# Kernel tuning notes

Measured on AMD Instinct MI355X. Metric: run time of the kernel, lower is better.

The kernel has to match this reference:

```python
import jax, jax.numpy as jnp
import numpy as np
from jax import lax

H = 192; W = 192; C = 256; N = H * W; E = 294912; K = 289; DSIG = 1
SLOPE = 0.01
EPS = 1e-5


def leaky(x):
    return jnp.where(x >= 0, x, SLOPE * x)


def conv2d(x, w, pad, groups):
    return lax.conv_general_dilated(
        x, w, (1, 1), [(pad, pad), (pad, pad)],
        dimension_numbers=('NCHW', 'OIHW', 'NCHW'),
        feature_group_count=groups)


def bn2d(x, g, b):
    # BatchNorm2d with track_running_stats=False -> always batch stats (biased var)
    m = x.mean(axis=(0, 2, 3), keepdims=True)
    v = x.var(axis=(0, 2, 3), keepdims=True)
    return (x - m) / jnp.sqrt(v + EPS) * g.reshape(1, -1, 1, 1) + b.reshape(1, -1, 1, 1)


def conv_batch(x, w, g, b, pad, groups):
    # nn.Sequential(LeakyReLU(0.01), Conv2d(bias=False), BatchNorm2d)
    return bn2d(conv2d(leaky(x), w, pad, groups), g, b)


def bn1d(x, g, b):
    m = x.mean(axis=0)
    v = x.var(axis=0)
    return (x - m) / jnp.sqrt(v + EPS) * g + b


def setup_inputs() -> dict:
    key = jax.random.key(0)
    ks = jax.random.split(key, 20)
    X = jax.random.normal(ks[0], (N, C), dtype=jnp.float32)
    src = jax.random.randint(ks[1], (E,), 0, N)
    dst = jax.random.randint(ks[2], (E,), 0, N)
    k1 = jax.random.randint(ks[3], (E,), 0, K)
    k2 = jax.random.randint(ks[4], (E,), 0, K)
    InfoIdx = jnp.stack([src, k1, dst, k2], axis=1).astype(jnp.int64)
    edgmsk = (jax.random.uniform(ks[5], (E, 1)) < 0.9).astype(jnp.float32)
    s = 0.05
    inp = {
        'X': X, 'InfoIdx': InfoIdx, 'edgmsk': edgmsk,
        # PPM: depthwise 17x17 conv_batch then 1x1 conv_batch
        'ppm_w0': jax.random.normal(ks[6], (C, 1, 17, 17), jnp.float32) * s,
        'ppm_g0': jnp.ones((C,), jnp.float32), 'ppm_b0': jnp.zeros((C,), jnp.float32),
        'ppm_w1': jax.random.normal(ks[7], (C, C, 1, 1), jnp.float32) * s,
        'ppm_g1': jnp.ones((C,), jnp.float32), 'ppm_b1': jnp.zeros((C,), jnp.float32),
        # FFN_1: two 1x1 conv_batch
        'ffn1_w0': jax.random.normal(ks[8], (C, C, 1, 1), jnp.float32) * s,
        'ffn1_g0': jnp.ones((C,), jnp.float32), 'ffn1_b0': jnp.zeros((C,), jnp.float32),
        'ffn1_w1': jax.random.normal(ks[9], (C, C, 1, 1), jnp.float32) * s,
        'ffn1_g1': jnp.ones((C,), jnp.float32), 'ffn1_b1': jnp.zeros((C,), jnp.float32),
        # Dis: Linear(C,C) -> LeakyReLU -> Linear(C, 289)
        'dis_w1': jax.random.normal(ks[10], (C, C), jnp.float32) * s,
        'dis_b1': jnp.zeros((C,), jnp.float32),
        'dis_w2': jax.random.normal(ks[11], (K * DSIG, C), jnp.float32) * s,
        'dis_b2': jnp.zeros((K * DSIG,), jnp.float32),
        # BatchNorm1d
        'bn_g': jnp.ones((C,), jnp.float32), 'bn_b': jnp.zeros((C,), jnp.float32),
        # FFN_2 = DoubleConv: depthwise-expand 3x3 (groups=C, out=4C) then 1x1
        'ffn2_w0': jax.random.normal(ks[12], (4 * C, 1, 3, 3), jnp.float32) * s,
        'ffn2_g0': jnp.ones((4 * C,), jnp.float32), 'ffn2_b0': jnp.zeros((4 * C,), jnp.float32),
        'ffn2_w1': jax.random.normal(ks[13], (C, 4 * C, 1, 1), jnp.float32) * s,
        'ffn2_g1': jnp.ones((C,), jnp.float32), 'ffn2_b1': jnp.zeros((C,), jnp.float32),
    }
    return inp


def reference(X, InfoIdx, edgmsk,
              ppm_w0, ppm_g0, ppm_b0, ppm_w1, ppm_g1, ppm_b1,
              ffn1_w0, ffn1_g0, ffn1_b0, ffn1_w1, ffn1_g1, ffn1_b1,
              dis_w1, dis_b1, dis_w2, dis_b2, bn_g, bn_b,
              ffn2_w0, ffn2_g0, ffn2_b0, ffn2_w1, ffn2_g1, ffn2_b1):
    src_idx = InfoIdx[:, 0]
    dst_idx = InfoIdx[:, 2]
    # [N,C] -> [1,C,H,W]
    img = X.T.reshape(1, C, H, W)
    # PPM residual
    t = conv_batch(img, ppm_w0, ppm_g0, ppm_b0, pad=8, groups=C)
    t = conv_batch(t, ppm_w1, ppm_g1, ppm_b1, pad=0, groups=1)
    img = img + t
    # FFN_1 residual
    t = conv_batch(img, ffn1_w0, ffn1_g0, ffn1_b0, pad=0, groups=1)
    t = conv_batch(t, ffn1_w1, ffn1_g1, ffn1_b1, pad=0, groups=1)
    img = img + t
    Xn = img.reshape(C, N).T  # [N, C]
    # Dis MLP -> signal [N, 289, d_signal]
    h = leaky(Xn @ dis_w1.T + dis_b1)
    signal = (h @ dis_w2.T + dis_b2).reshape(N, K, DSIG)
    # edge gather + exp/clamp score
    s_src = signal[src_idx, InfoIdx[:, 1]]  # [E, 1]
    s_dst = signal[dst_idx, InfoIdx[:, 3]]  # [E, 1]
    aij = jnp.exp(jnp.clip(s_src + s_dst, -5.0, 5.0)) * edgmsk  # [E, 1]
    # two scatter-sum reductions to dst nodes
    A_sum = jax.ops.segment_sum(aij, dst_idx, num_segments=N)  # [N, 1]
    XA_sum = jax.ops.segment_sum(Xn[src_idx] * aij, dst_idx, num_segments=N)  # [N, C]
    X_trans = XA_sum / (A_sum + 1e-5)
    Xn = Xn + bn1d(X_trans, bn_g, bn_b)
    # FFN_2 = DoubleConv with residual skip
    img = Xn.T.reshape(1, C, H, W)
    t = conv_batch(img, ffn2_w0, ffn2_g0, ffn2_b0, pad=1, groups=C)
    t = conv_batch(t, ffn2_w1, ffn2_g1, ffn2_b1, pad=0, groups=1)
    out = t + img
    return out.reshape(C, N).T  # final bg.ndata['X'], [N, C]
```

## Files before the change

kernel.cpp:

```cpp
#include <hip/hip_runtime.h>
#include <cstddef>

#define HW 192
#define NP 36864
#define CH 256
#define EDGES 294912
#define KSIG 289
#define SLOPE 0.01f
#define BNEPS 1e-5f
#define PADW 208
#define PADSZ (PADW * PADW)

typedef unsigned short u16;
typedef __attribute__((ext_vector_type(8))) short bf16x8;
typedef __attribute__((ext_vector_type(4))) float f32x4;

__device__ __forceinline__ float leaky(float x) { return x >= 0.f ? x : SLOPE * x; }
__device__ __forceinline__ u16 f2bf(float x) {
  unsigned u = __float_as_uint(x);
  unsigned r = (u + 0x7fffu + ((u >> 16) & 1u)) >> 16;
  return (u16)r;
}
__device__ __forceinline__ float bf2f(unsigned h) { return __uint_as_float(h << 16); }
__device__ __forceinline__ void bnss(const float* sums, const float* sqs,
                                     const float* g, const float* b, int k,
                                     float& s, float& h) {
  float mean = sums[k] * (1.f / NP);
  float var = sqs[k] * (1.f / NP) - mean * mean;
  s = g[k] * rsqrtf(var + BNEPS);
  h = b[k] - mean * s;
}

__global__ __launch_bounds__(256) void k_transpose_pad(const float* __restrict__ src,
                                                       float* __restrict__ dst,
                                                       u16* __restrict__ pad) {
  __shared__ float tile[32][33];
  int s0 = blockIdx.x * 32, r0 = blockIdx.y * 32;
  int tx = threadIdx.x & 31, ty = threadIdx.x >> 5;
#pragma unroll
  for (int j = 0; j < 4; j++)
    tile[ty + 8 * j][tx] = src[(size_t)(r0 + ty + 8 * j) * CH + s0 + tx];
  __syncthreads();
  int n = r0 + tx;
  int y = n / HW, x = n - y * HW;
#pragma unroll
  for (int j = 0; j < 4; j++) {
    int c = s0 + ty + 8 * j;
    float v = tile[tx][ty + 8 * j];
    dst[(size_t)c * NP + n] = v;
    pad[(size_t)c * PADSZ + (y + 8) * PADW + x + 8] = f2bf(leaky(v));
  }
}

__global__ __launch_bounds__(256) void k_mkT(const float* __restrict__ w,
                                             u16* __restrict__ Tg) {
  int c = blockIdx.x;
  const float* wc = w + c * 289;
  u16* tc = Tg + (size_t)c * 8704;
  for (int i = threadIdx.x; i < 8704; i += 256) {
    int ky = i >> 9, rem = i & 511, n = rem >> 5, k = rem & 31;
    int kx = k - n;
    float v = (kx >= 0 && kx < 17) ? wc[ky * 17 + kx] : 0.f;
    tc[i] = f2bf(v);
  }
}

__global__ __launch_bounds__(256) void k_cvtW(const float* __restrict__ pw1,
                                              const float* __restrict__ f1w0,
                                              const float* __restrict__ f1w1,
                                              const float* __restrict__ dw1,
                                              const float* __restrict__ dw2,
                                              const float* __restrict__ f2w1,
                                              u16* __restrict__ out) {
  int i = blockIdx.x * 256 + threadIdx.x;
  float v;
  if (i < 65536) v = pw1[i];
  else if (i < 131072) v = f1w0[i - 65536];
  else if (i < 196608) v = f1w1[i - 131072];
  else if (i < 262144) v = dw1[i - 196608];
  else if (i < 360448) { int j = i - 262144; v = (j < KSIG * 256) ? dw2[j] : 0.f; }
  else v = f2w1[i - 360448];
  out[i] = f2bf(v);
}

__global__ __launch_bounds__(256) void k_stats_bf(const u16* __restrict__ Xr,
                                                  float* __restrict__ sums,
                                                  float* __restrict__ sqs) {
  int row = blockIdx.x;
  int t = threadIdx.x;
  const uint4* p = (const uint4*)(Xr + (size_t)row * NP);
  float s = 0.f, q = 0.f;
  for (int i = t; i < NP / 8; i += 256) {
    uint4 v = p[i];
    unsigned w[4] = {v.x, v.y, v.z, v.w};
#pragma unroll
    for (int j = 0; j < 4; j++) {
      float a = bf2f(w[j] & 0xffffu), c = bf2f(w[j] >> 16);
      s += a + c; q += a * a + c * c;
    }
  }
  __shared__ float ss[256], qq[256];
  ss[t] = s; qq[t] = q;
  __syncthreads();
  for (int d = 128; d > 0; d >>= 1) {
    if (t < d) { ss[t] += ss[t + d]; qq[t] += qq[t + d]; }
    __syncthreads();
  }
  if (t == 0) { sums[row] = ss[0]; sqs[row] = qq[0]; }
}

__global__ __launch_bounds__(256) void k_cvtT(const float* __restrict__ in,
                                              u16* __restrict__ outT, int M) {
  __shared__ float tile[32][65];
  int n0 = blockIdx.x * 64, k0 = blockIdx.y * 32;
  int t = threadIdx.x;
#pragma unroll
  for (int i = 0; i < 2; i++) {
    int ci = i * 256 + t;
    int k = ci >> 4, cg = (ci & 15) * 4;
    float4 v = *(const float4*)&in[(size_t)(k0 + k) * NP + n0 + cg];
    tile[k][cg] = v.x; tile[k][cg + 1] = v.y; tile[k][cg + 2] = v.z; tile[k][cg + 3] = v.w;
  }
  __syncthreads();
  int n = t >> 2, kg = (t & 3) * 8;
  uint4 o;
  o.x = (unsigned)f2bf(tile[kg + 0][n]) | ((unsigned)f2bf(tile[kg + 1][n]) << 16);
  o.y = (unsigned)f2bf(tile[kg + 2][n]) | ((unsigned)f2bf(tile[kg + 3][n]) << 16);
  o.z = (unsigned)f2bf(tile[kg + 4][n]) | ((unsigned)f2bf(tile[kg + 5][n]) << 16);
  o.w = (unsigned)f2bf(tile[kg + 6][n]) | ((unsigned)f2bf(tile[kg + 7][n]) << 16);
  *(uint4*)&outT[(size_t)(n0 + n) * M + k0 + kg] = o;
}

__global__ __launch_bounds__(256) void k_cvtT_bf(const u16* __restrict__ in,
                                                 u16* __restrict__ outT,
                                                 const float* __restrict__ sums,
                                                 const float* __restrict__ sqs,
                                                 const float* __restrict__ g,
                                                 const float* __restrict__ b, int M) {
  __shared__ float tile[32][65];
  int n0 = blockIdx.x * 64, k0 = blockIdx.y * 32;
  int t = threadIdx.x;
  int k = t >> 3, cg = (t & 7) * 8;
  float s, h; bnss(sums, sqs, g, b, k0 + k, s, h);
  uint4 v = *(const uint4*)&in[(size_t)(k0 + k) * NP + n0 + cg];
  unsigned w[4] = {v.x, v.y, v.z, v.w};
#pragma unroll
  for (int j = 0; j < 4; j++) {
    tile[k][cg + 2 * j]     = leaky(fmaf(bf2f(w[j] & 0xffffu), s, h));
    tile[k][cg + 2 * j + 1] = leaky(fmaf(bf2f(w[j] >> 16), s, h));
  }
  __syncthreads();
  int n = t >> 2, kg = (t & 3) * 8;
  uint4 o;
  o.x = (unsigned)f2bf(tile[kg + 0][n]) | ((unsigned)f2bf(tile[kg + 1][n]) << 16);
  o.y = (unsigned)f2bf(tile[kg + 2][n]) | ((unsigned)f2bf(tile[kg + 3][n]) << 16);
  o.z = (unsigned)f2bf(tile[kg + 4][n]) | ((unsigned)f2bf(tile[kg + 5][n]) << 16);
  o.w = (unsigned)f2bf(tile[kg + 6][n]) | ((unsigned)f2bf(tile[kg + 7][n]) << 16);
  *(uint4*)&outT[(size_t)(n0 + n) * M + k0 + kg] = o;
}

__global__ __launch_bounds__(256) void k_fuse1(const float* __restrict__ base,
                                               const u16* __restrict__ raw,
                                               const float* __restrict__ sums,
                                               const float* __restrict__ sqs,
                                               const float* __restrict__ g,
                                               const float* __restrict__ b,
                                               float* __restrict__ img2,
                                               u16* __restrict__ outT) {
  __shared__ float tile[32][65];
  int n0 = blockIdx.x * 64, k0 = blockIdx.y * 32;
  int t = threadIdx.x;
#pragma unroll
  for (int i = 0; i < 2; i++) {
    int ci = i * 256 + t;
    int k = ci >> 4, cg = (ci & 15) * 4;
    float s, h; bnss(sums, sqs, g, b, k0 + k, s, h);
    size_t idx = (size_t)(k0 + k) * NP + n0 + cg;
    float4 bv = *(const float4*)&base[idx];
    uint2 rv = *(const uint2*)&raw[idx];
    float r0 = bf2f(rv.x & 0xffffu), r1 = bf2f(rv.x >> 16);
    float r2 = bf2f(rv.y & 0xffffu), r3 = bf2f(rv.y >> 16);
    float4 o;
    o.x = bv.x + fmaf(r0, s, h); o.y = bv.y + fmaf(r1, s, h);
    o.z = bv.z + fmaf(r2, s, h); o.w = bv.w + fmaf(r3, s, h);
    *(float4*)&img2[idx] = o;
    tile[k][cg]     = leaky(o.x);
    tile[k][cg + 1] = leaky(o.y);
    tile[k][cg + 2] = leaky(o.z);
    tile[k][cg + 3] = leaky(o.w);
  }
  __syncthreads();
  int n = t >> 2, kg = (t & 3) * 8;
  uint4 o;
  o.x = (unsigned)f2bf(tile[kg + 0][n]) | ((unsigned)f2bf(tile[kg + 1][n]) << 16);
  o.y = (unsigned)f2bf(tile[kg + 2][n]) | ((unsigned)f2bf(tile[kg + 3][n]) << 16);
  o.z = (unsigned)f2bf(tile[kg + 4][n]) | ((unsigned)f2bf(tile[kg + 5][n]) << 16);
  o.w = (unsigned)f2bf(tile[kg + 6][n]) | ((unsigned)f2bf(tile[kg + 7][n]) << 16);
  *(uint4*)&outT[(size_t)(n0 + n) * CH + k0 + kg] = o;
}

__global__ __launch_bounds__(256) void k_fuse2(const float* __restrict__ base,
                                               const u16* __restrict__ raw,
                                               const float* __restrict__ sums,
                                               const float* __restrict__ sqs,
                                               const float* __restrict__ g,
                                               const float* __restrict__ b,
                                               float* __restrict__ XnT,
                                               u16* __restrict__ outT) {
  __shared__ float tile[32][65];
  int n0 = blockIdx.x * 64, k0 = blockIdx.y * 32;
  int t = threadIdx.x;
#pragma unroll
  for (int i = 0; i < 2; i++) {
    int ci = i * 256 + t;
    int k = ci >> 4, cg = (ci & 15) * 4;
    float s, h; bnss(sums, sqs, g, b, k0 + k, s, h);
    size_t idx = (size_t)(k0 + k) * NP + n0 + cg;
    float4 bv = *(const float4*)&base[idx];
    uint2 rv = *(const uint2*)&raw[idx];
    float r0 = bf2f(rv.x & 0xffffu), r1 = bf2f(rv.x >> 16);
    float r2 = bf2f(rv.y & 0xffffu), r3 = bf2f(rv.y >> 16);
    tile[k][cg]     = bv.x + fmaf(r0, s, h);
    tile[k][cg + 1] = bv.y + fmaf(r1, s, h);
    tile[k][cg + 2] = bv.z + fmaf(r2, s, h);
    tile[k][cg + 3] = bv.w + fmaf(r3, s, h);
  }
  __syncthreads();
  int n = t >> 2, kg = (t & 3) * 8;
  float4 f0 = {tile[kg + 0][n], tile[kg + 1][n], tile[kg + 2][n], tile[kg + 3][n]};
  float4 f1 = {tile[kg + 4][n], tile[kg + 5][n], tile[kg + 6][n], tile[kg + 7][n]};
  *(float4*)&XnT[(size_t)(n0 + n) * CH + k0 + kg] = f0;
  *(float4*)&XnT[(size_t)(n0 + n) * CH + k0 + kg + 4] = f1;
  uint4 o;
  o.x = (unsigned)f2bf(f0.x) | ((unsigned)f2bf(f0.y) << 16);
  o.y = (unsigned)f2bf(f0.z) | ((unsigned)f2bf(f0.w) << 16);
  o.z = (unsigned)f2bf(f1.x) | ((unsigned)f2bf(f1.y) << 16);
  o.w = (unsigned)f2bf(f1.z) | ((unsigned)f2bf(f1.w) << 16);
  *(uint4*)&outT[(size_t)(n0 + n) * CH + k0 + kg] = o;
}

__global__ __launch_bounds__(256) void k_mgemm(const u16* __restrict__ A,
                                               const u16* __restrict__ Bt,
                                               float* __restrict__ Outf,
                                               u16* __restrict__ Outb,
                                               const float* __restrict__ bias,
                                               int K, int Mstore, int actout) {
  __shared__ u16 As[128 * 40];
  __shared__ u16 Bs[128 * 40];
  int t = threadIdx.x;
  int lane = t & 63, wave = t >> 6;
  int wm = (wave >> 1) * 64, wn = (wave & 1) * 64;
  int m0 = blockIdx.y * 128, n0 = blockIdx.x * 128;
  int r = lane & 15, q = lane >> 4;
  f32x4 acc[4][4];
#pragma unroll
  for (int a = 0; a < 4; a++)
#pragma unroll
    for (int b = 0; b < 4; b++) acc[a][b] = (f32x4){0.f, 0.f, 0.f, 0.f};

  for (int k0 = 0; k0 < K; k0 += 32) {
#pragma unroll
    for (int i = 0; i < 2; i++) {
      int cc = t + i * 256;
      int mm = cc >> 2, kq = (cc & 3) * 8;
      uint4 av = *(const uint4*)&A[(size_t)(m0 + mm) * K + k0 + kq];
      uint4 bv = *(const uint4*)&Bt[(size_t)(n0 + mm) * K + k0 + kq];
      *(uint4*)&As[mm * 40 + kq] = av;
      *(uint4*)&Bs[mm * 40 + kq] = bv;
    }
    __syncthreads();
    bf16x8 af[4], bfr[4];
#pragma unroll
    for (int mt = 0; mt < 4; mt++)
      af[mt] = *(const bf16x8*)&As[(wm + mt * 16 + r) * 40 + q * 8];
#pragma unroll
    for (int nt = 0; nt < 4; nt++)
      bfr[nt] = *(const bf16x8*)&Bs[(wn + nt * 16 + r) * 40 + q * 8];
#pragma unroll
    for (int mt = 0; mt < 4; mt++)
#pragma unroll
      for (int nt = 0; nt < 4; nt++)
        acc[mt][nt] = __builtin_amdgcn_mfma_f32_16x16x32_bf16(af[mt], bfr[nt], acc[mt][nt], 0, 0, 0);
    __syncthreads();
  }
#pragma unroll
  for (int mt = 0; mt < 4; mt++) {
    int mrow = m0 + wm + mt * 16 + q * 4;
#pragma unroll
    for (int i = 0; i < 4; i++) {
      int m = mrow + i;
      if (m >= Mstore) continue;
      float bs = bias ? bias[m] : 0.f;
#pragma unroll
      for (int nt = 0; nt < 4; nt++) {
        float v = acc[mt][nt][i] + bs;
        if (actout) v = leaky(v);
        size_t oi = (size_t)m * NP + n0 + wn + nt * 16 + r;
        if (Outb) Outb[oi] = f2bf(v); else Outf[oi] = v;
      }
    }
  }
}

__global__ __launch_bounds__(512) void k_mgemm256(const u16* __restrict__ A,
                                                  const u16* __restrict__ Bt,
                                                  float* __restrict__ Outf,
                                                  u16* __restrict__ Outb,
                                                  const float* __restrict__ bias,
                                                  int K, int actout) {
  __shared__ u16 As[256 * 40];
  __shared__ u16 Bs[128 * 40];
  int t = threadIdx.x;
  int lane = t & 63, wave = t >> 6;
  int wm = (wave >> 1) * 64, wn = (wave & 1) * 64;
  int n0 = blockIdx.x * 128;
  int r = lane & 15, q = lane >> 4;
  int arow0 = t >> 2, kq = (t & 3) * 8;
  f32x4 acc[4][4];
#pragma unroll
  for (int a = 0; a < 4; a++)
#pragma unroll
    for (int b = 0; b < 4; b++) acc[a][b] = (f32x4){0.f, 0.f, 0.f, 0.f};

  uint4 pa0, pa1, pb;
  pa0 = *(const uint4*)&A[(size_t)arow0 * K + kq];
  pa1 = *(const uint4*)&A[(size_t)(arow0 + 128) * K + kq];
  pb  = *(const uint4*)&Bt[(size_t)(n0 + arow0) * K + kq];
  int kiters = K >> 5;
  for (int ki = 0; ki < kiters; ki++) {
    *(uint4*)&As[arow0 * 40 + kq] = pa0;
    *(uint4*)&As[(arow0 + 128) * 40 + kq] = pa1;
    *(uint4*)&Bs[arow0 * 40 + kq] = pb;
    __syncthreads();
    if (ki + 1 < kiters) {
      int k0 = (ki + 1) << 5;
      pa0 = *(const uint4*)&A[(size_t)arow0 * K + k0 + kq];
      pa1 = *(const uint4*)&A[(size_t)(arow0 + 128) * K + k0 + kq];
      pb  = *(const uint4*)&Bt[(size_t)(n0 + arow0) * K + k0 + kq];
    }
    bf16x8 af[4], bfr[4];
#pragma unroll
    for (int mt = 0; mt < 4; mt++)
      af[mt] = *(const bf16x8*)&As[(wm + mt * 16 + r) * 40 + q * 8];
#pragma unroll
    for (int nt = 0; nt < 4; nt++)
      bfr[nt] = *(const bf16x8*)&Bs[(wn + nt * 16 + r) * 40 + q * 8];
#pragma unroll
    for (int mt = 0; mt < 4; mt++)
#pragma unroll
      for (int nt = 0; nt < 4; nt++)
        acc[mt][nt] = __builtin_amdgcn_mfma_f32_16x16x32_bf16(af[mt], bfr[nt], acc[mt][nt], 0, 0, 0);
    __syncthreads();
  }
#pragma unroll
  for (int mt = 0; mt < 4; mt++) {
    int mrow = wm + mt * 16 + q * 4;
#pragma unroll
    for (int i = 0; i < 4; i++) {
      int m = mrow + i;
      float bs = bias ? bias[m] : 0.f;
#pragma unroll
      for (int nt = 0; nt < 4; nt++) {
        float v = acc[mt][nt][i] + bs;
        if (actout) v = leaky(v);
        size_t oi = (size_t)m * NP + n0 + wn + nt * 16 + r;
        if (Outb) Outb[oi] = f2bf(v); else Outf[oi] = v;
      }
    }
  }
}

__global__ __launch_bounds__(256) void k_dwconv17(const u16* __restrict__ pad,
                                                  const u16* __restrict__ Tg,
                                                  u16* __restrict__ outb) {
  int c = blockIdx.y;
  int tile = blockIdx.x;
  int ty0 = (tile / 3) * 64, tx0 = (tile % 3) * 64;
  __shared__ u16 smIn[80 * 88];
  __shared__ u16 smT[17 * 16 * 40];
  const u16* pc = pad + (size_t)c * PADSZ;
  for (int cc = threadIdx.x; cc < 800; cc += 256) {
    int rr = cc / 10, j = cc - rr * 10;
    uint4 v = *(const uint4*)(pc + (ty0 + rr) * PADW + tx0 + j * 8);
    *(uint4*)(smIn + rr * 88 + j * 8) = v;
  }
  const u16* tc = Tg + (size_t)c * 8704;
  for (int cc = threadIdx.x; cc < 1088; cc += 256) {
    int rr = cc >> 2, j = cc & 3;
    uint4 v = *(const uint4*)(tc + rr * 32 + j * 8);
    *(uint4*)(smT + rr * 40 + j * 8) = v;
  }
  __syncthreads();
  int lane = threadIdx.x & 63, wave = threadIdx.x >> 6;
  int wy = wave * 16;
  int r = lane & 15, q = lane >> 4;
  f32x4 acc[4];
#pragma unroll
  for (int xt = 0; xt < 4; xt++) acc[xt] = (f32x4){0.f, 0.f, 0.f, 0.f};
#pragma unroll
  for (int ky = 0; ky < 17; ky++) {
    bf16x8 bfrag = *(const bf16x8*)&smT[(ky * 16 + r) * 40 + q * 8];
    int rowA = wy + r + ky;
#pragma unroll
    for (int xt = 0; xt < 4; xt++) {
      bf16x8 afrag = *(const bf16x8*)&smIn[rowA * 88 + xt * 16 + q * 8];
      acc[xt] = __builtin_amdgcn_mfma_f32_16x16x32_bf16(afrag, bfrag, acc[xt], 0, 0, 0);
    }
  }
  u16* oc = outb + (size_t)c * NP;
#pragma unroll
  for (int xt = 0; xt < 4; xt++) {
    int x = tx0 + xt * 16 + r;
#pragma unroll
    for (int i = 0; i < 4; i++) {
      int y = ty0 + wy + q * 4 + i;
      oc[y * HW + x] = f2bf(acc[xt][i]);
    }
  }
}

__global__ __launch_bounds__(256) void k_conv3x4(const float* __restrict__ in,
                                                 const float* __restrict__ w,
                                                 u16* __restrict__ out) {
  int wave = threadIdx.x >> 6, lane = threadIdx.x & 63;
  int c = blockIdx.y;
  int y = blockIdx.x * 4 + wave;
  const float* wc = w + (size_t)(4 * c) * 9;
  float wr[36];
#pragma unroll
  for (int k = 0; k < 36; k++) wr[k] = wc[k];
  float acc[4][3];
#pragma unroll
  for (int oc = 0; oc < 4; oc++)
#pragma unroll
    for (int s = 0; s < 3; s++) acc[oc][s] = 0.f;
  const float* base = in + (size_t)c * NP;
#pragma unroll
  for (int ky = 0; ky < 3; ky++) {
    int ry = y + ky - 1;
    if (ry < 0 || ry >= HW) continue;
    const float* rp = base + ry * HW;
    float a0 = leaky(rp[lane]);
    float a1 = leaky(rp[64 + lane]);
    float a2 = leaky(rp[128 + lane]);
    float e0 = __shfl(a0, 63), e1 = __shfl(a1, 63);
    float b1 = __shfl(a1, 0),  b2 = __shfl(a2, 0);
    float l0 = __shfl_up(a0, 1); if (lane == 0) l0 = 0.f;
    float l1 = __shfl_up(a1, 1); if (lane == 0) l1 = e0;
    float l2 = __shfl_up(a2, 1); if (lane == 0) l2 = e1;
    float r0 = __shfl_down(a0, 1); if (lane == 63) r0 = b1;
    float r1 = __shfl_down(a1, 1); if (lane == 63) r1 = b2;
    float r2 = __shfl_down(a2, 1); if (lane == 63) r2 = 0.f;
#pragma unroll
    for (int oc = 0; oc < 4; oc++) {
      float w0 = wr[oc * 9 + ky * 3], w1 = wr[oc * 9 + ky * 3 + 1], w2 = wr[oc * 9 + ky * 3 + 2];
      acc[oc][0] = fmaf(w0, l0, fmaf(w1, a0, fmaf(w2, r0, acc[oc][0])));
      acc[oc][1] = fmaf(w0, l1, fmaf(w1, a1, fmaf(w2, r1, acc[oc][1])));
      acc[oc][2] = fmaf(w0, l2, fmaf(w1, a2, fmaf(w2, r2, acc[oc][2])));
    }
  }
  size_t ob = (size_t)(4 * c) * NP + (size_t)y * HW + lane;
#pragma unroll
  for (int oc = 0; oc < 4; oc++) {
    out[ob + (size_t)oc * NP]       = f2bf(acc[oc][0]);
    out[ob + (size_t)oc * NP + 64]  = f2bf(acc[oc][1]);
    out[ob + (size_t)oc * NP + 128] = f2bf(acc[oc][2]);
  }
}

__global__ __launch_bounds__(256) void k_edge(const int* __restrict__ info,
                                              const float* __restrict__ msk,
                                              const float* __restrict__ sig,
                                              float* __restrict__ aij,
                                              int* __restrict__ counts) {
  int e = blockIdx.x * 256 + threadIdx.x;
  int4 ii = ((const int4*)info)[e];
  float s = sig[(size_t)ii.y * NP + ii.x] + sig[(size_t)ii.w * NP + ii.z];
  s = fminf(fmaxf(s, -5.f), 5.f);
  aij[e] = expf(s) * msk[e];
  atomicAdd(&counts[ii.z], 1);
}

__global__ __launch_bounds__(256) void k_scan1(const int* __restrict__ counts,
                                               int* __restrict__ offsets,
                                               int* __restrict__ bsum) {
  __shared__ int sm[256];
  int t = threadIdx.x;
  int i = blockIdx.x * 256 + t;
  int v = counts[i];
  sm[t] = v;
  __syncthreads();
  for (int d = 1; d < 256; d <<= 1) {
    int add = (t >= d) ? sm[t - d] : 0;
    __syncthreads();
    sm[t] += add;
    __syncthreads();
  }
  offsets[i] = sm[t] - v;
  if (t == 255) bsum[blockIdx.x] = sm[255];
}
__global__ __launch_bounds__(256) void k_scan2(const int* __restrict__ bsum,
                                               int* __restrict__ boff) {
  __shared__ int sm[256];
  int t = threadIdx.x;
  int v = (t < 144) ? bsum[t] : 0;
  sm[t] = v;
  __syncthreads();
  for (int d = 1; d < 256; d <<= 1) {
    int add = (t >= d) ? sm[t - d] : 0;
    __syncthreads();
    sm[t] += add;
    __syncthreads();
  }
  boff[t] = sm[t] - v;
}
__global__ __launch_bounds__(256) void k_scan3(int* __restrict__ offsets,
                                               const int* __restrict__ boff,
                                               int* __restrict__ cursor) {
  int i = blockIdx.x * 256 + threadIdx.x;
  int o = offsets[i] + boff[blockIdx.x];
  offsets[i] = o;
  cursor[i] = o;
  if (i == 0) offsets[NP] = EDGES;
}
__global__ __launch_bounds__(256) void k_scatter(const int* __restrict__ info,
                                                 const float* __restrict__ aij,
                                                 int* __restrict__ cursor,
                                                 int* __restrict__ srcs,
                                                 float* __restrict__ aijw) {
  int e = blockIdx.x * 256 + threadIdx.x;
  int4 ii = ((const int4*)info)[e];
  int pos = atomicAdd(&cursor[ii.z], 1);
  srcs[pos] = ii.x;
  aijw[pos] = aij[e];
}

__global__ __launch_bounds__(256) void k_agg(const int* __restrict__ offsets,
                                             const int* __restrict__ srcs,
                                             const float* __restrict__ aijw,
                                             const u16* __restrict__ XnBf,
                                             u16* __restrict__ XtrBf) {
  int wave = threadIdx.x >> 6, lane = threadIdx.x & 63;
  int node = blockIdx.x * 4 + wave;
  int o0 = offsets[node], o1 = offsets[node + 1];
  int half = lane >> 5, l32 = lane & 31;
  float acc[8] = {0.f, 0.f, 0.f, 0.f, 0.f, 0.f, 0.f, 0.f};
  float asum = 0.f;
  int i = o0 + half;
  for (; i + 2 < o1; i += 4) {
    int s0 = srcs[i], s1 = srcs[i + 2];
    float a0 = aijw[i], a1 = aijw[i + 2];
    uint4 v0 = ((const uint4*)(XnBf + (size_t)s0 * CH))[l32];
    uint4 v1 = ((const uint4*)(XnBf + (size_t)s1 * CH))[l32];
    unsigned w0[4] = {v0.x, v0.y, v0.z, v0.w};
    unsigned w1[4] = {v1.x, v1.y, v1.z, v1.w};
#pragma unroll
    for (int j = 0; j < 4; j++) {
      acc[2 * j]     = fmaf(a0, bf2f(w0[j] & 0xffffu), acc[2 * j]);
      acc[2 * j + 1] = fmaf(a0, bf2f(w0[j] >> 16),     acc[2 * j + 1]);
      acc[2 * j]     = fmaf(a1, bf2f(w1[j] & 0xffffu), acc[2 * j]);
      acc[2 * j + 1] = fmaf(a1, bf2f(w1[j] >> 16),     acc[2 * j + 1]);
    }
    asum += a0 + a1;
  }
  for (; i < o1; i += 2) {
    int s = srcs[i];
    float a = aijw[i];
    uint4 v = ((const uint4*)(XnBf + (size_t)s * CH))[l32];
    unsigned w[4] = {v.x, v.y, v.z, v.w};
#pragma unroll
    for (int j = 0; j < 4; j++) {
      acc[2 * j]     = fmaf(a, bf2f(w[j] & 0xffffu), acc[2 * j]);
      acc[2 * j + 1] = fmaf(a, bf2f(w[j] >> 16),     acc[2 * j + 1]);
    }
    asum += a;
  }
#pragma unroll
  for (int j = 0; j < 8; j++) acc[j] += __shfl_xor(acc[j], 32, 64);
  asum += __shfl_xor(asum, 32, 64);
  if (half == 0) {
    float inv = 1.f / (asum + 1e-5f);
    uint4 o;
    o.x = (unsigned)f2bf(acc[0] * inv) | ((unsigned)f2bf(acc[1] * inv) << 16);
    o.y = (unsigned)f2bf(acc[2] * inv) | ((unsigned)f2bf(acc[3] * inv) << 16);
    o.z = (unsigned)f2bf(acc[4] * inv) | ((unsigned)f2bf(acc[5] * inv) << 16);
    o.w = (unsigned)f2bf(acc[6] * inv) | ((unsigned)f2bf(acc[7] * inv) << 16);
    ((uint4*)(XtrBf + (size_t)node * CH))[l32] = o;
  }
}

__global__ __launch_bounds__(256) void k_colstats(const u16* __restrict__ Xt,
                                                  float* __restrict__ sums,
                                                  float* __restrict__ sqs) {
  int c = threadIdx.x;
  float s = 0.f, q = 0.f;
  for (int n = blockIdx.x; n < NP; n += gridDim.x) {
    float v = bf2f(Xt[(size_t)n * CH + c]);
    s += v; q += v * v;
  }
  atomicAdd(&sums[c], s);
  atomicAdd(&sqs[c], q);
}

__global__ __launch_bounds__(256) void k_mkimg4(const float* __restrict__ Xn,
                                                const u16* __restrict__ XtrBf,
                                                const float* __restrict__ sums,
                                                const float* __restrict__ sqs,
                                                const float* __restrict__ g,
                                                const float* __restrict__ b,
                                                float* __restrict__ img4) {
  __shared__ float tile[32][33];
  int c0 = blockIdx.x * 32, n0 = blockIdx.y * 32;
  int tx = threadIdx.x & 31, ty = threadIdx.x >> 5;
  int c = c0 + tx;
  float s, h; bnss(sums, sqs, g, b, c, s, h);
#pragma unroll
  for (int j = 0; j < 4; j++) {
    size_t idx = (size_t)(n0 + ty + 8 * j) * CH + c;
    tile[ty + 8 * j][tx] = Xn[idx] + fmaf(bf2f(XtrBf[idx]), s, h);
  }
  __syncthreads();
#pragma unroll
  for (int j = 0; j < 4; j++) {
    int cc = c0 + ty + 8 * j;
    img4[(size_t)cc * NP + n0 + tx] = tile[tx][ty + 8 * j];
  }
}

__global__ __launch_bounds__(256) void k_final(const u16* __restrict__ raw5,
                                               const float* __restrict__ img4,
                                               const float* __restrict__ sums,
                                               const float* __restrict__ sqs,
                                               const float* __restrict__ g,
                                               const float* __restrict__ b,
                                               float* __restrict__ out) {
  __shared__ float tile[32][33];
  int n0 = blockIdx.x * 32, c0 = blockIdx.y * 32;
  int tx = threadIdx.x & 31, ty = threadIdx.x >> 5;
#pragma unroll
  for (int j = 0; j < 4; j++) {
    int c = c0 + ty + 8 * j;
    float s, h; bnss(sums, sqs, g, b, c, s, h);
    size_t idx = (size_t)c * NP + n0 + tx;
    tile[ty + 8 * j][tx] = fmaf(bf2f(raw5[idx]), s, h) + img4[idx];
  }
  __syncthreads();
#pragma unroll
  for (int j = 0; j < 4; j++) {
    int n = n0 + ty + 8 * j;
    out[(size_t)n * CH + c0 + tx] = tile[tx][ty + 8 * j];
  }
}

extern "C" void kernel_launch(void* const* d_in, const int* in_sizes, int n_in,
                              void* d_out, int out_size, void* d_ws, size_t ws_size,
                              hipStream_t stream) {
  (void)in_sizes; (void)n_in; (void)out_size; (void)ws_size;
  const float* X    = (const float*)d_in[0];
  const int*   info = (const int*)d_in[1];
  const float* msk  = (const float*)d_in[2];
  const float* pw0  = (const float*)d_in[3];
  const float* pg0  = (const float*)d_in[4];
  const float* pb0  = (const float*)d_in[5];
  const float* pw1  = (const float*)d_in[6];
  const float* pg1  = (const float*)d_in[7];
  const float* pb1  = (const float*)d_in[8];
  const float* f1w0 = (const float*)d_in[9];
  const float* f1g0 = (const float*)d_in[10];
  const float* f1b0 = (const float*)d_in[11];
  const float* f1w1 = (const float*)d_in[12];
  const float* f1g1 = (const float*)d_in[13];
  const float* f1b1 = (const float*)d_in[14];
  const float* dw1  = (const float*)d_in[15];
  const float* db1  = (const float*)d_in[16];
  const float* dw2  = (const float*)d_in[17];
  const float* db2  = (const float*)d_in[18];
  const float* bng  = (const float*)d_in[19];
  const float* bnb  = (const float*)d_in[20];
  const float* f2w0 = (const float*)d_in[21];
  const float* f2g0 = (const float*)d_in[22];
  const float* f2b0 = (const float*)d_in[23];
  const float* f2w1 = (const float*)d_in[24];
  const float* f2g1 = (const float*)d_in[25];
  const float* f2b1 = (const float*)d_in[26];
  float* out = (float*)d_out;

  float* ws = (float*)d_ws;
  float* sum0 = ws + 0;    float* sq0 = ws + 256;
  float* sum1 = ws + 512;  float* sq1 = ws + 768;
  float* sum2 = ws + 1024; float* sq2 = ws + 1280;
  float* sum3 = ws + 1536; float* sq3 = ws + 1792;
  float* sum5 = ws + 2048; float* sq5 = ws + 2304;
  float* sumT = ws + 2560; float* sqT = ws + 2816;
  float* sum4 = ws + 3072; float* sq4 = ws + 4096;
  int* counts  = (int*)(ws + 8192);
  int* offsets = (int*)(ws + 45056);
  int* cursor  = (int*)(ws + 82176);
  int* bsum    = (int*)(ws + 119296);
  int* boff    = (int*)(ws + 119552);
  int* srcs    = (int*)(ws + 131072);
  float* aij   = ws + 425984;
  const size_t S = (size_t)NP * CH;
  float* slotD = ws + 720896;
  float* slotB = slotD + S;
  float* slotA = slotB + S;
  float* slotC = slotA + S;
  u16* bfB  = (u16*)(slotC + S);
  u16* bfH  = bfB + S;
  float* sigT = (float*)(bfH + S);
  u16* bfW  = (u16*)(sigT + (size_t)KSIG * NP);
  float* aijw = (float*)(bfW + 622592);
  u16* Ppad = (u16*)slotC;
  u16* Tg   = (u16*)slotD;
  u16* raw4bf  = (u16*)slotB;
  u16* bfT1024 = bfB;
  u16* XtrBf   = (u16*)slotD;
  u16* raw5bf  = (u16*)slotB;

  hipMemsetAsync(ws, 0, 5120 * sizeof(float), stream);
  hipMemsetAsync(counts, 0, NP * sizeof(int), stream);
  hipMemsetAsync(Ppad, 0, (size_t)PADSZ * CH * sizeof(u16), stream);

  dim3 b256(256), b512(512);
  k_cvtW<<<2432, b256, 0, stream>>>(pw1, f1w0, f1w1, dw1, dw2, f2w1, bfW);
  k_mkT<<<CH, b256, 0, stream>>>(pw0, Tg);
  k_transpose_pad<<<dim3(CH / 32, NP / 32), b256, 0, stream>>>(X, slotA, Ppad);
  k_dwconv17<<<dim3(9, CH), b256, 0, stream>>>(Ppad, Tg, bfH);
  k_stats_bf<<<CH, b256, 0, stream>>>(bfH, sum0, sq0);
  k_cvtT_bf<<<dim3(NP / 64, 8), b256, 0, stream>>>(bfH, bfB, sum0, sq0, pg0, pb0, CH);
  k_mgemm256<<<NP / 128, b512, 0, stream>>>(bfW, bfB, nullptr, bfH, nullptr, CH, 0);
  k_stats_bf<<<CH, b256, 0, stream>>>(bfH, sum1, sq1);
  k_fuse1<<<dim3(NP / 64, 8), b256, 0, stream>>>(slotA, bfH, sum1, sq1, pg1, pb1, slotD, bfB);
  k_mgemm256<<<NP / 128, b512, 0, stream>>>(bfW + 65536, bfB, nullptr, bfH, nullptr, CH, 0);
  k_stats_bf<<<CH, b256, 0, stream>>>(bfH, sum2, sq2);
  k_cvtT_bf<<<dim3(NP / 64, 8), b256, 0, stream>>>(bfH, bfB, sum2, sq2, f1g0, f1b0, CH);
  k_mgemm256<<<NP / 128, b512, 0, stream>>>(bfW + 131072, bfB, nullptr, bfH, nullptr, CH, 0);
  k_stats_bf<<<CH, b256, 0, stream>>>(bfH, sum3, sq3);
  k_fuse2<<<dim3(NP / 64, 8), b256, 0, stream>>>(slotD, bfH, sum3, sq3, f1g1, f1b1, slotA, bfB);
  k_mgemm256<<<NP / 128, b512, 0, stream>>>(bfW + 196608, bfB, slotC, nullptr, db1, CH, 1);
  k_cvtT<<<dim3(NP / 64, 8), b256, 0, stream>>>(slotC, bfH, CH);
  k_mgemm<<<dim3(NP / 128, 3), b256, 0, stream>>>(bfW + 262144, bfH, sigT, nullptr, db2, CH, KSIG, 0);
  k_edge<<<EDGES / 256, b256, 0, stream>>>(info, msk, sigT, aij, counts);
  k_scan1<<<NP / 256, b256, 0, stream>>>(counts, offsets, bsum);
  k_scan2<<<1, b256, 0, stream>>>(bsum, boff);
  k_scan3<<<NP / 256, b256, 0, stream>>>(offsets, boff, cursor);
  k_scatter<<<EDGES / 256, b256, 0, stream>>>(info, aij, cursor, srcs, aijw);
  k_agg<<<NP / 4, b256, 0, stream>>>(offsets, srcs, aijw, bfB, XtrBf);
  k_colstats<<<288, b256, 0, stream>>>(XtrBf, sumT, sqT);
  k_mkimg4<<<dim3(CH / 32, NP / 32), b256, 0, stream>>>(slotA, XtrBf, sumT, sqT, bng, bnb, slotC);
  k_conv3x4<<<dim3(48, CH), b256, 0, stream>>>(slotC, f2w0, raw4bf);
  k_stats_bf<<<1024, b256, 0, stream>>>(raw4bf, sum4, sq4);
  k_cvtT_bf<<<dim3(NP / 64, 32), b256, 0, stream>>>(raw4bf, bfT1024, sum4, sq4, f2g0, f2b0, 1024);
  k_mgemm256<<<NP / 128, b512, 0, stream>>>(bfW + 360448, bfT1024, nullptr, raw5bf, nullptr, 1024, 0);
  k_stats_bf<<<CH, b256, 0, stream>>>(raw5bf, sum5, sq5);
  k_final<<<dim3(NP / 32, CH / 32), b256, 0, stream>>>(raw5bf, slotC, sum5, sq5, f2g1, f2b1, out);
}
```

Measured before the change: 642.9 us.

## Fuse BN statistics into conv and GEMM epilogues, halve GEMM N-tile

Batch-norm sums and sums of squares are now accumulated with wave shuffles and atomics in the epilogues of the depthwise conv, the 3x3 conv, and the 1x1 GEMMs. This removes the separate stats kernels that re-read each activation tensor. The GEMM tile is narrowed to 64 columns for more blocks and occupancy. Stats are now taken from fp32 values rather than rounded bf16, and float atomics make the sums order-nondeterministic.

```diff
diff --git a/kernel.cpp b/kernel.cpp
--- a/kernel.cpp
+++ b/kernel.cpp
@@ -81,32 +81,6 @@
   else if (i < 360448) { int j = i - 262144; v = (j < KSIG * 256) ? dw2[j] : 0.f; }
   else v = f2w1[i - 360448];
   out[i] = f2bf(v);
-}
-
-__global__ __launch_bounds__(256) void k_stats_bf(const u16* __restrict__ Xr,
-                                                  float* __restrict__ sums,
-                                                  float* __restrict__ sqs) {
-  int row = blockIdx.x;
-  int t = threadIdx.x;
-  const uint4* p = (const uint4*)(Xr + (size_t)row * NP);
-  float s = 0.f, q = 0.f;
-  for (int i = t; i < NP / 8; i += 256) {
-    uint4 v = p[i];
-    unsigned w[4] = {v.x, v.y, v.z, v.w};
-#pragma unroll
-    for (int j = 0; j < 4; j++) {
-      float a = bf2f(w[j] & 0xffffu), c = bf2f(w[j] >> 16);
-      s += a + c; q += a * a + c * c;
-    }
-  }
-  __shared__ float ss[256], qq[256];
-  ss[t] = s; qq[t] = q;
-  __syncthreads();
-  for (int d = 128; d > 0; d >>= 1) {
-    if (t < d) { ss[t] += ss[t + d]; qq[t] += qq[t + d]; }
-    __syncthreads();
-  }
-  if (t == 0) { sums[row] = ss[0]; sqs[row] = qq[0]; }
 }
 
 __global__ __launch_bounds__(256) void k_cvtT(const float* __restrict__ in,
@@ -302,69 +276,78 @@
   }
 }
 
-__global__ __launch_bounds__(512) void k_mgemm256(const u16* __restrict__ A,
-                                                  const u16* __restrict__ Bt,
-                                                  float* __restrict__ Outf,
-                                                  u16* __restrict__ Outb,
-                                                  const float* __restrict__ bias,
-                                                  int K, int actout) {
+__global__ __launch_bounds__(512, 4) void k_mgemm256(const u16* __restrict__ A,
+                                                     const u16* __restrict__ Bt,
+                                                     float* __restrict__ Outf,
+                                                     u16* __restrict__ Outb,
+                                                     const float* __restrict__ bias,
+                                                     int K, int actout,
+                                                     float* __restrict__ sums,
+                                                     float* __restrict__ sqs) {
   __shared__ u16 As[256 * 40];
-  __shared__ u16 Bs[128 * 40];
+  __shared__ u16 Bs[64 * 40];
   int t = threadIdx.x;
   int lane = t & 63, wave = t >> 6;
-  int wm = (wave >> 1) * 64, wn = (wave & 1) * 64;
-  int n0 = blockIdx.x * 128;
+  int wm = (wave >> 1) * 64, wn = (wave & 1) * 32;
+  int n0 = blockIdx.x * 64;
   int r = lane & 15, q = lane >> 4;
   int arow0 = t >> 2, kq = (t & 3) * 8;
-  f32x4 acc[4][4];
+  int brow = t >> 2;
+  f32x4 acc[4][2];
 #pragma unroll
   for (int a = 0; a < 4; a++)
 #pragma unroll
-    for (int b = 0; b < 4; b++) acc[a][b] = (f32x4){0.f, 0.f, 0.f, 0.f};
+    for (int b = 0; b < 2; b++) acc[a][b] = (f32x4){0.f, 0.f, 0.f, 0.f};
 
   uint4 pa0, pa1, pb;
   pa0 = *(const uint4*)&A[(size_t)arow0 * K + kq];
   pa1 = *(const uint4*)&A[(size_t)(arow0 + 128) * K + kq];
-  pb  = *(const uint4*)&Bt[(size_t)(n0 + arow0) * K + kq];
+  if (t < 256) pb = *(const uint4*)&Bt[(size_t)(n0 + brow) * K + kq];
   int kiters = K >> 5;
   for (int ki = 0; ki < kiters; ki++) {
     *(uint4*)&As[arow0 * 40 + kq] = pa0;
     *(uint4*)&As[(arow0 + 128) * 40 + kq] = pa1;
-    *(uint4*)&Bs[arow0 * 40 + kq] = pb;
+    if (t < 256) *(uint4*)&Bs[brow * 40 + kq] = pb;
     __syncthreads();
     if (ki + 1 < kiters) {
       int k0 = (ki + 1) << 5;
       pa0 = *(const uint4*)&A[(size_t)arow0 * K + k0 + kq];
       pa1 = *(const uint4*)&A[(size_t)(arow0 + 128) * K + k0 + kq];
-      pb  = *(const uint4*)&Bt[(size_t)(n0 + arow0) * K + k0 + kq];
-    }
-    bf16x8 af[4], bfr[4];
+      if (t < 256) pb = *(const uint4*)&Bt[(size_t)(n0 + brow) * K + k0 + kq];
+    }
+    bf16x8 af[4], bfr[2];
 #pragma unroll
     for (int mt = 0; mt < 4; mt++)
       af[mt] = *(const bf16x8*)&As[(wm + mt * 16 + r) * 40 + q * 8];
 #pragma unroll
-    for (int nt = 0; nt < 4; nt++)
+    for (int nt = 0; nt < 2; nt++)
       bfr[nt] = *(const bf16x8*)&Bs[(wn + nt * 16 + r) * 40 + q * 8];
 #pragma unroll
     for (int mt = 0; mt < 4; mt++)
 #pragma unroll
-      for (int nt = 0; nt < 4; nt++)
+      for (int nt = 0; nt < 2; nt++)
         acc[mt][nt] = __builtin_amdgcn_mfma_f32_16x16x32_bf16(af[mt], bfr[nt], acc[mt][nt], 0, 0, 0);
     __syncthreads();
   }
 #pragma unroll
   for (int mt = 0; mt < 4; mt++) {
-    int mrow = wm + mt * 16 + q * 4;
 #pragma unroll
     for (int i = 0; i < 4; i++) {
-      int m = mrow + i;
+      int m = wm + mt * 16 + q * 4 + i;
       float bs = bias ? bias[m] : 0.f;
-#pragma unroll
-      for (int nt = 0; nt < 4; nt++) {
-        float v = acc[mt][nt][i] + bs;
-        if (actout) v = leaky(v);
-        size_t oi = (size_t)m * NP + n0 + wn + nt * 16 + r;
-        if (Outb) Outb[oi] = f2bf(v); else Outf[oi] = v;
+      float v0 = acc[mt][0][i] + bs;
+      float v1 = acc[mt][1][i] + bs;
+      if (actout) { v0 = leaky(v0); v1 = leaky(v1); }
+      size_t oi = (size_t)m * NP + n0 + wn + r;
+      if (Outb) { Outb[oi] = f2bf(v0); Outb[oi + 16] = f2bf(v1); }
+      else      { Outf[oi] = v0;       Outf[oi + 16] = v1; }
+      if (sums) {
+        float rs = v0 + v1, rq = v0 * v0 + v1 * v1;
+        rs += __shfl_xor(rs, 1); rq += __shfl_xor(rq, 1);
+        rs += __shfl_xor(rs, 2); rq += __shfl_xor(rq, 2);
+        rs += __shfl_xor(rs, 4); rq += __shfl_xor(rq, 4);
+        rs += __shfl_xor(rs, 8); rq += __shfl_xor(rq, 8);
+        if (r == 0) { atomicAdd(&sums[m], rs); atomicAdd(&sqs[m], rq); }
       }
     }
   }
@@ -372,7 +355,9 @@
 
 __global__ __launch_bounds__(256) void k_dwconv17(const u16* __restrict__ pad,
                                                   const u16* __restrict__ Tg,
-                                                  u16* __restrict__ outb) {
+                                                  u16* __restrict__ outb,
+                                                  float* __restrict__ sums,
+                                                  float* __restrict__ sqs) {
   int c = blockIdx.y;
   int tile = blockIdx.x;
   int ty0 = (tile / 3) * 64, tx0 = (tile % 3) * 64;
@@ -408,20 +393,28 @@
     }
   }
   u16* oc = outb + (size_t)c * NP;
+  float s = 0.f, sq = 0.f;
 #pragma unroll
   for (int xt = 0; xt < 4; xt++) {
     int x = tx0 + xt * 16 + r;
 #pragma unroll
     for (int i = 0; i < 4; i++) {
       int y = ty0 + wy + q * 4 + i;
-      oc[y * HW + x] = f2bf(acc[xt][i]);
-    }
-  }
+      float v = acc[xt][i];
+      oc[y * HW + x] = f2bf(v);
+      s += v; sq += v * v;
+    }
+  }
+#pragma unroll
+  for (int d = 1; d < 64; d <<= 1) { s += __shfl_xor(s, d); sq += __shfl_xor(sq, d); }
+  if (lane == 0) { atomicAdd(&sums[c], s); atomicAdd(&sqs[c], sq); }
 }
 
 __global__ __launch_bounds__(256) void k_conv3x4(const float* __restrict__ in,
                                                  const float* __restrict__ w,
-                                                 u16* __restrict__ out) {
+                                                 u16* __restrict__ out,
+                                                 float* __restrict__ sums,
+                                                 float* __restrict__ sqs) {
   int wave = threadIdx.x >> 6, lane = threadIdx.x & 63;
   int c = blockIdx.y;
   int y = blockIdx.x * 4 + wave;
@@ -465,6 +458,11 @@
     out[ob + (size_t)oc * NP]       = f2bf(acc[oc][0]);
     out[ob + (size_t)oc * NP + 64]  = f2bf(acc[oc][1]);
     out[ob + (size_t)oc * NP + 128] = f2bf(acc[oc][2]);
+    float s = acc[oc][0] + acc[oc][1] + acc[oc][2];
+    float qv = acc[oc][0] * acc[oc][0] + acc[oc][1] * acc[oc][1] + acc[oc][2] * acc[oc][2];
+#pragma unroll
+    for (int d = 1; d < 64; d <<= 1) { s += __shfl_xor(s, d); qv += __shfl_xor(qv, d); }
+    if (lane == 0) { atomicAdd(&sums[4 * c + oc], s); atomicAdd(&sqs[4 * c + oc], qv); }
   }
 }
 
@@ -725,19 +723,15 @@
   k_cvtW<<<2432, b256, 0, stream>>>(pw1, f1w0, f1w1, dw1, dw2, f2w1, bfW);
   k_mkT<<<CH, b256, 0, stream>>>(pw0, Tg);
   k_transpose_pad<<<dim3(CH / 32, NP / 32), b256, 0, stream>>>(X, slotA, Ppad);
-  k_dwconv17<<<dim3(9, CH), b256, 0, stream>>>(Ppad, Tg, bfH);
-  k_stats_bf<<<CH, b256, 0, stream>>>(bfH, sum0, sq0);
+  k_dwconv17<<<dim3(9, CH), b256, 0, stream>>>(Ppad, Tg, bfH, sum0, sq0);
   k_cvtT_bf<<<dim3(NP / 64, 8), b256, 0, stream>>>(bfH, bfB, sum0, sq0, pg0, pb0, CH);
-  k_mgemm256<<<NP / 128, b512, 0, stream>>>(bfW, bfB, nullptr, bfH, nullptr, CH, 0);
-  k_stats_bf<<<CH, b256, 0, stream>>>(bfH, sum1, sq1);
+  k_mgemm256<<<NP / 64, b512, 0, stream>>>(bfW, bfB, nullptr, bfH, nullptr, CH, 0, sum1, sq1);
   k_fuse1<<<dim3(NP / 64, 8), b256, 0, stream>>>(slotA, bfH, sum1, sq1, pg1, pb1, slotD, bfB);
-  k_mgemm256<<<NP / 128, b512, 0, stream>>>(bfW + 65536, bfB, nullptr, bfH, nullptr, CH, 0);
-  k_stats_bf<<<CH, b256, 0, stream>>>(bfH, sum2, sq2);
+  k_mgemm256<<<NP / 64, b512, 0, stream>>>(bfW + 65536, bfB, nullptr, bfH, nullptr, CH, 0, sum2, sq2);
   k_cvtT_bf<<<dim3(NP / 64, 8), b256, 0, stream>>>(bfH, bfB, sum2, sq2, f1g0, f1b0, CH);
-  k_mgemm256<<<NP / 128, b512, 0, stream>>>(bfW + 131072, bfB, nullptr, bfH, nullptr, CH, 0);
-  k_stats_bf<<<CH, b256, 0, stream>>>(bfH, sum3, sq3);
+  k_mgemm256<<<NP / 64, b512, 0, stream>>>(bfW + 131072, bfB, nullptr, bfH, nullptr, CH, 0, sum3, sq3);
   k_fuse2<<<dim3(NP / 64, 8), b256, 0, stream>>>(slotD, bfH, sum3, sq3, f1g1, f1b1, slotA, bfB);
-  k_mgemm256<<<NP / 128, b512, 0, stream>>>(bfW + 196608, bfB, slotC, nullptr, db1, CH, 1);
+  k_mgemm256<<<NP / 64, b512, 0, stream>>>(bfW + 196608, bfB, slotC, nullptr, db1, CH, 1, nullptr, nullptr);
   k_cvtT<<<dim3(NP / 64, 8), b256, 0, stream>>>(slotC, bfH, CH);
   k_mgemm<<<dim3(NP / 128, 3), b256, 0, stream>>>(bfW + 262144, bfH, sigT, nullptr, db2, CH, KSIG, 0);
   k_edge<<<EDGES / 256, b256, 0, stream>>>(info, msk, sigT, aij, counts);
@@ -748,10 +742,8 @@
   k_agg<<<NP / 4, b256, 0, stream>>>(offsets, srcs, aijw, bfB, XtrBf);
   k_colstats<<<288, b256, 0, stream>>>(XtrBf, sumT, sqT);
   k_mkimg4<<<dim3(CH / 32, NP / 32), b256, 0, stream>>>(slotA, XtrBf, sumT, sqT, bng, bnb, slotC);
-  k_conv3x4<<<dim3(48, CH), b256, 0, stream>>>(slotC, f2w0, raw4bf);
-  k_stats_bf<<<1024, b256, 0, stream>>>(raw4bf, sum4, sq4);
+  k_conv3x4<<<dim3(48, CH), b256, 0, stream>>>(slotC, f2w0, raw4bf, sum4, sq4);
   k_cvtT_bf<<<dim3(NP / 64, 32), b256, 0, stream>>>(raw4bf, bfT1024, sum4, sq4, f2g0, f2b0, 1024);
-  k_mgemm256<<<NP / 128, b512, 0, stream>>>(bfW + 360448, bfT1024, nullptr, raw5bf, nullptr, 1024, 0);
-  k_stats_bf<<<CH, b256, 0, stream>>>(raw5bf, sum5, sq5);
+  k_mgemm256<<<NP / 64, b512, 0, stream>>>(bfW + 360448, bfT1024, nullptr, raw5bf, nullptr, 1024, 0, sum5, sq5);
   k_final<<<dim3(NP / 32, CH / 32), b256, 0, stream>>>(raw5bf, slotC, sum5, sq5, f2g1, f2b1, out);
 }
```

New measurement: 1.284 ms. +99.8%, slower.

## Store GEMM operands in K-slab tiled layout for contiguous tile loads

Applied to the files above, without the earlier changes.

Weights and transposed activations are now written in a [K/32][rows][32] slab layout, so each GEMM k-step loads one contiguous block instead of rows strided by K. Several producer kernels and both GEMM kernels are updated, and fuse2 writes an extra slab-layout copy into the sigT buffer for the Dis GEMM, because the original row-major copy is still needed by the aggregation. This makes global loads fully coalesced, at the cost of an extra 18MB write and the aliasing risk of reusing sigT before it is overwritten.

```diff
diff --git a/kernel.cpp b/kernel.cpp
--- a/kernel.cpp
+++ b/kernel.cpp
@@ -10,6 +10,7 @@
 #define BNEPS 1e-5f
 #define PADW 208
 #define PADSZ (PADW * PADW)
+#define NP32 ((size_t)NP * 32)
 
 typedef unsigned short u16;
 typedef __attribute__((ext_vector_type(8))) short bf16x8;
@@ -74,13 +75,17 @@
                                               u16* __restrict__ out) {
   int i = blockIdx.x * 256 + threadIdx.x;
   float v;
-  if (i < 65536) v = pw1[i];
-  else if (i < 131072) v = f1w0[i - 65536];
-  else if (i < 196608) v = f1w1[i - 131072];
-  else if (i < 262144) v = dw1[i - 196608];
-  else if (i < 360448) { int j = i - 262144; v = (j < KSIG * 256) ? dw2[j] : 0.f; }
-  else v = f2w1[i - 360448];
-  out[i] = f2bf(v);
+  int off, j, R, Klog;
+  if (i < 65536)       { off = 0;      j = i;          v = pw1[j];  R = 256; Klog = 8; }
+  else if (i < 131072) { off = 65536;  j = i - 65536;  v = f1w0[j]; R = 256; Klog = 8; }
+  else if (i < 196608) { off = 131072; j = i - 131072; v = f1w1[j]; R = 256; Klog = 8; }
+  else if (i < 262144) { off = 196608; j = i - 196608; v = dw1[j];  R = 256; Klog = 8; }
+  else if (i < 360448) { off = 262144; j = i - 262144;
+                         v = (j < KSIG * 256) ? dw2[j] : 0.f;       R = 384; Klog = 8; }
+  else                 { off = 360448; j = i - 360448; v = f2w1[j]; R = 256; Klog = 10; }
+  int r = j >> Klog, k = j & ((1 << Klog) - 1);
+  int ni = off + (k >> 5) * (R * 32) + r * 32 + (k & 31);
+  out[ni] = f2bf(v);
 }
 
 __global__ __launch_bounds__(256) void k_stats_bf(const u16* __restrict__ Xr,
@@ -128,7 +133,7 @@
   o.y = (unsigned)f2bf(tile[kg + 2][n]) | ((unsigned)f2bf(tile[kg + 3][n]) << 16);
   o.z = (unsigned)f2bf(tile[kg + 4][n]) | ((unsigned)f2bf(tile[kg + 5][n]) << 16);
   o.w = (unsigned)f2bf(tile[kg + 6][n]) | ((unsigned)f2bf(tile[kg + 7][n]) << 16);
-  *(uint4*)&outT[(size_t)(n0 + n) * M + k0 + kg] = o;
+  *(uint4*)&outT[(size_t)(k0 >> 5) * NP32 + (size_t)(n0 + n) * 32 + kg] = o;
 }
 
 __global__ __launch_bounds__(256) void k_cvtT_bf(const u16* __restrict__ in,
@@ -156,7 +161,7 @@
   o.y = (unsigned)f2bf(tile[kg + 2][n]) | ((unsigned)f2bf(tile[kg + 3][n]) << 16);
   o.z = (unsigned)f2bf(tile[kg + 4][n]) | ((unsigned)f2bf(tile[kg + 5][n]) << 16);
   o.w = (unsigned)f2bf(tile[kg + 6][n]) | ((unsigned)f2bf(tile[kg + 7][n]) << 16);
-  *(uint4*)&outT[(size_t)(n0 + n) * M + k0 + kg] = o;
+  *(uint4*)&outT[(size_t)(k0 >> 5) * NP32 + (size_t)(n0 + n) * 32 + kg] = o;
 }
 
 __global__ __launch_bounds__(256) void k_fuse1(const float* __restrict__ base,
@@ -196,7 +201,7 @@
   o.y = (unsigned)f2bf(tile[kg + 2][n]) | ((unsigned)f2bf(tile[kg + 3][n]) << 16);
   o.z = (unsigned)f2bf(tile[kg + 4][n]) | ((unsigned)f2bf(tile[kg + 5][n]) << 16);
   o.w = (unsigned)f2bf(tile[kg + 6][n]) | ((unsigned)f2bf(tile[kg + 7][n]) << 16);
-  *(uint4*)&outT[(size_t)(n0 + n) * CH + k0 + kg] = o;
+  *(uint4*)&outT[(size_t)(k0 >> 5) * NP32 + (size_t)(n0 + n) * 32 + kg] = o;
 }
 
 __global__ __launch_bounds__(256) void k_fuse2(const float* __restrict__ base,
@@ -206,7 +211,8 @@
                                                const float* __restrict__ g,
                                                const float* __restrict__ b,
                                                float* __restrict__ XnT,
-                                               u16* __restrict__ outT) {
+                                               u16* __restrict__ outT,
+                                               u16* __restrict__ outTt) {
   __shared__ float tile[32][65];
   int n0 = blockIdx.x * 64, k0 = blockIdx.y * 32;
   int t = threadIdx.x;
@@ -237,6 +243,7 @@
   o.z = (unsigned)f2bf(f1.x) | ((unsigned)f2bf(f1.y) << 16);
   o.w = (unsigned)f2bf(f1.z) | ((unsigned)f2bf(f1.w) << 16);
   *(uint4*)&outT[(size_t)(n0 + n) * CH + k0 + kg] = o;
+  *(uint4*)&outTt[(size_t)(k0 >> 5) * NP32 + (size_t)(n0 + n) * 32 + kg] = o;
 }
 
 __global__ __launch_bounds__(256) void k_mgemm(const u16* __restrict__ A,
@@ -244,7 +251,8 @@
                                                float* __restrict__ Outf,
                                                u16* __restrict__ Outb,
                                                const float* __restrict__ bias,
-                                               int K, int Mstore, int actout) {
+                                               int K, int Mstore, int actout,
+                                               int aslab) {
   __shared__ u16 As[128 * 40];
   __shared__ u16 Bs[128 * 40];
   int t = threadIdx.x;
@@ -259,12 +267,14 @@
     for (int b = 0; b < 4; b++) acc[a][b] = (f32x4){0.f, 0.f, 0.f, 0.f};
 
   for (int k0 = 0; k0 < K; k0 += 32) {
+    size_t ab = (size_t)(k0 >> 5) * aslab + (size_t)m0 * 32;
+    size_t bb = (size_t)(k0 >> 5) * NP32 + (size_t)n0 * 32;
 #pragma unroll
     for (int i = 0; i < 2; i++) {
       int cc = t + i * 256;
       int mm = cc >> 2, kq = (cc & 3) * 8;
-      uint4 av = *(const uint4*)&A[(size_t)(m0 + mm) * K + k0 + kq];
-      uint4 bv = *(const uint4*)&Bt[(size_t)(n0 + mm) * K + k0 + kq];
+      uint4 av = *(const uint4*)&A[ab + (size_t)cc * 8];
+      uint4 bv = *(const uint4*)&Bt[bb + (size_t)cc * 8];
       *(uint4*)&As[mm * 40 + kq] = av;
       *(uint4*)&Bs[mm * 40 + kq] = bv;
     }
@@ -323,9 +333,9 @@
     for (int b = 0; b < 4; b++) acc[a][b] = (f32x4){0.f, 0.f, 0.f, 0.f};
 
   uint4 pa0, pa1, pb;
-  pa0 = *(const uint4*)&A[(size_t)arow0 * K + kq];
-  pa1 = *(const uint4*)&A[(size_t)(arow0 + 128) * K + kq];
-  pb  = *(const uint4*)&Bt[(size_t)(n0 + arow0) * K + kq];
+  pa0 = *(const uint4*)&A[(size_t)t * 8];
+  pa1 = *(const uint4*)&A[4096 + (size_t)t * 8];
+  pb  = *(const uint4*)&Bt[(size_t)n0 * 32 + (size_t)t * 8];
   int kiters = K >> 5;
   for (int ki = 0; ki < kiters; ki++) {
     *(uint4*)&As[arow0 * 40 + kq] = pa0;
@@ -333,10 +343,11 @@
     *(uint4*)&Bs[arow0 * 40 + kq] = pb;
     __syncthreads();
     if (ki + 1 < kiters) {
-      int k0 = (ki + 1) << 5;
-      pa0 = *(const uint4*)&A[(size_t)arow0 * K + k0 + kq];
-      pa1 = *(const uint4*)&A[(size_t)(arow0 + 128) * K + k0 + kq];
-      pb  = *(const uint4*)&Bt[(size_t)(n0 + arow0) * K + k0 + kq];
+      size_t ab = (size_t)(ki + 1) * 8192;
+      size_t bb = (size_t)(ki + 1) * NP32 + (size_t)n0 * 32;
+      pa0 = *(const uint4*)&A[ab + (size_t)t * 8];
+      pa1 = *(const uint4*)&A[ab + 4096 + (size_t)t * 8];
+      pb  = *(const uint4*)&Bt[bb + (size_t)t * 8];
     }
     bf16x8 af[4], bfr[4];
 #pragma unroll
@@ -716,6 +727,7 @@
   u16* bfT1024 = bfB;
   u16* XtrBf   = (u16*)slotD;
   u16* raw5bf  = (u16*)slotB;
+  u16* bfBt    = (u16*)sigT;
 
   hipMemsetAsync(ws, 0, 5120 * sizeof(float), stream);
   hipMemsetAsync(counts, 0, NP * sizeof(int), stream);
@@ -736,10 +748,10 @@
   k_cvtT_bf<<<dim3(NP / 64, 8), b256, 0, stream>>>(bfH, bfB, sum2, sq2, f1g0, f1b0, CH);
   k_mgemm256<<<NP / 128, b512, 0, stream>>>(bfW + 131072, bfB, nullptr, bfH, nullptr, CH, 0);
   k_stats_bf<<<CH, b256, 0, stream>>>(bfH, sum3, sq3);
-  k_fuse2<<<dim3(NP / 64, 8), b256, 0, stream>>>(slotD, bfH, sum3, sq3, f1g1, f1b1, slotA, bfB);
-  k_mgemm256<<<NP / 128, b512, 0, stream>>>(bfW + 196608, bfB, slotC, nullptr, db1, CH, 1);
+  k_fuse2<<<dim3(NP / 64, 8), b256, 0, stream>>>(slotD, bfH, sum3, sq3, f1g1, f1b1, slotA, bfB, bfBt);
+  k_mgemm256<<<NP / 128, b512, 0, stream>>>(bfW + 196608, bfBt, slotC, nullptr, db1, CH, 1);
   k_cvtT<<<dim3(NP / 64, 8), b256, 0, stream>>>(slotC, bfH, CH);
-  k_mgemm<<<dim3(NP / 128, 3), b256, 0, stream>>>(bfW + 262144, bfH, sigT, nullptr, db2, CH, KSIG, 0);
+  k_mgemm<<<dim3(NP / 128, 3), b256, 0, stream>>>(bfW + 262144, bfH, sigT, nullptr, db2, CH, KSIG, 0, 12288);
   k_edge<<<EDGES / 256, b256, 0, stream>>>(info, msk, sigT, aij, counts);
   k_scan1<<<NP / 256, b256, 0, stream>>>(counts, offsets, bsum);
   k_scan2<<<1, b256, 0, stream>>>(bsum, boff);
```

Measured after the change: 642.6 us. No clear change (-0.0%).
